# Optimization experiments

Measured on AMD Instinct MI355X. Metric: run time of the kernel, lower is better.

The kernel has to match this reference:

```python
import jax, jax.numpy as jnp
import numpy as np

D_MODEL = 2048
NUM_HEADS = 16
D_K = D_MODEL // NUM_HEADS
B, S, PAST = 2, 1024, 3072


def setup_inputs() -> dict:
    key = jax.random.key(0)
    ks = jax.random.split(key, 12)
    s = 1.0 / np.sqrt(D_MODEL)
    inp = {
        "x": jax.random.normal(ks[0], (B, S, D_MODEL), dtype=jnp.float32),
        "past_key": jax.random.normal(ks[1], (B, NUM_HEADS, PAST, D_K), dtype=jnp.float32),
        "past_value": jax.random.normal(ks[2], (B, NUM_HEADS, PAST, D_K), dtype=jnp.float32),
        "Wq": jax.random.normal(ks[3], (D_MODEL, D_MODEL), dtype=jnp.float32) * s,
        "bq": jax.random.normal(ks[4], (D_MODEL,), dtype=jnp.float32) * s,
        "Wk": jax.random.normal(ks[5], (D_MODEL, D_MODEL), dtype=jnp.float32) * s,
        "bk": jax.random.normal(ks[6], (D_MODEL,), dtype=jnp.float32) * s,
        "Wv": jax.random.normal(ks[7], (D_MODEL, D_MODEL), dtype=jnp.float32) * s,
        "bv": jax.random.normal(ks[8], (D_MODEL,), dtype=jnp.float32) * s,
        "Wo": jax.random.normal(ks[9], (D_MODEL, D_MODEL), dtype=jnp.float32) * s,
        "bo": jax.random.normal(ks[10], (D_MODEL,), dtype=jnp.float32) * s,
    }
    return inp


def reference(x, past_key, past_value, Wq, bq, Wk, bk, Wv, bv, Wo, bo):
    b, s, _ = x.shape
    # torch nn.Linear: y = x @ W^T + b
    def proj(W, bias):
        y = jnp.einsum('bsd,ed->bse', x, W) + bias
        return y.reshape(b, s, NUM_HEADS, D_K).transpose(0, 2, 1, 3)  # [B,H,S,dk]
    Q = proj(Wq, bq)
    K = proj(Wk, bk)
    V = proj(Wv, bv)
    K = jnp.concatenate([past_key, K], axis=2)   # [B,H,PAST+S,dk]
    V = jnp.concatenate([past_value, V], axis=2)
    scale = 1.0 / np.sqrt(D_K).astype(np.float32)
    scores = jnp.einsum('bhqd,bhkd->bhqk', Q, K) * scale
    attn = jax.nn.softmax(scores, axis=-1)
    out = jnp.einsum('bhqk,bhkd->bhqd', attn, V)          # [B,H,S,dk]
    out = out.transpose(0, 2, 1, 3).reshape(b, s, D_MODEL)
    out = jnp.einsum('bsd,ed->bse', out, Wo) + bo
    return out, K, V
```

## Files before the change

### kernel.cpp

```cpp
#include <hip/hip_runtime.h>
#include <stdint.h>

typedef __bf16 bf16;
typedef __bf16 bf16x4 __attribute__((ext_vector_type(4)));
typedef __bf16 bf16x8 __attribute__((ext_vector_type(8)));
typedef float  f32x4  __attribute__((ext_vector_type(4)));

#define DMODEL 2048
#define NH 16
#define DK 128
#define SS 1024
#define PASTLEN 3072
#define LTOT 4096
#define KVTILES 64
#define NSPLIT 4
#define NT 16

__device__ __forceinline__ void gload16(const void* g, void* l) {
    __builtin_amdgcn_global_load_lds(
        (__attribute__((address_space(1))) void*)(uintptr_t)g,
        (__attribute__((address_space(3))) void*)(uintptr_t)l,
        16, 0, 0);
}

__global__ __launch_bounds__(256) void cvt5_k(
    const float* __restrict__ s0, const float* __restrict__ s1,
    const float* __restrict__ s2, const float* __restrict__ s3,
    const float* __restrict__ s4,
    bf16* __restrict__ d0, bf16* __restrict__ d1, bf16* __restrict__ d2,
    bf16* __restrict__ d3, bf16* __restrict__ d4, int n8)
{
    const float* s; bf16* d;
    switch (blockIdx.y) {
        case 0: s = s0; d = d0; break;
        case 1: s = s1; d = d1; break;
        case 2: s = s2; d = d2; break;
        case 3: s = s3; d = d3; break;
        default: s = s4; d = d4; break;
    }
    int stride = gridDim.x * blockDim.x;
    for (int i = blockIdx.x*blockDim.x + threadIdx.x; i < n8; i += stride) {
        const float4* p = (const float4*)s + (size_t)i*2;
        float4 a = p[0], b = p[1];
        bf16x8 o;
        o[0]=(bf16)a.x; o[1]=(bf16)a.y; o[2]=(bf16)a.z; o[3]=(bf16)a.w;
        o[4]=(bf16)b.x; o[5]=(bf16)b.y; o[6]=(bf16)b.z; o[7]=(bf16)b.w;
        *((bf16x8*)d + i) = o;
    }
}

__global__ __launch_bounds__(256) void gemm_bt(
    const bf16* __restrict__ A,
    const bf16* __restrict__ W0, const bf16* __restrict__ W1, const bf16* __restrict__ W2,
    const float* __restrict__ b0, const float* __restrict__ b1, const float* __restrict__ b2,
    bf16* __restrict__ outQ, float* __restrict__ outK, float* __restrict__ outV,
    float* __restrict__ outO,
    const float* __restrict__ pk, const float* __restrict__ pv,
    bf16* __restrict__ Kbb, bf16* __restrict__ Vbb, int mode)
{
    __shared__ __align__(16) char lds[34816];
    const int tid  = threadIdx.x;

    if (mode == 0 && blockIdx.x >= 768) {
        float* Vt_f = (float*)lds;
        const int pp  = blockIdx.x - 768;
        const int tau = pp % 48, bh = pp / 48;
        const float* srcK = pk + ((size_t)bh*PASTLEN + tau*64)*DK;
        const float* srcV = pv + ((size_t)bh*PASTLEN + tau*64)*DK;
        float* dstKf = outK + ((size_t)bh*LTOT + tau*64)*DK;
        float* dstVf = outV + ((size_t)bh*LTOT + tau*64)*DK;
        char* kblob = (char*)Kbb + (((size_t)bh*KVTILES + tau) << 14);
        char* vblob = (char*)Vbb + (((size_t)bh*KVTILES + tau) << 14);
        #pragma unroll
        for (int i = 0; i < 8; ++i) {
            const int f4 = i*256 + tid;
            const int r  = f4 >> 5;
            const int c8 = f4 & 31;
            float4 k4 = ((const float4*)srcK)[f4];
            float4 v4 = ((const float4*)srcV)[f4];
            ((float4*)dstKf)[f4] = k4;
            ((float4*)dstVf)[f4] = v4;
            bf16x4 kq; kq[0]=(bf16)k4.x; kq[1]=(bf16)k4.y; kq[2]=(bf16)k4.z; kq[3]=(bf16)k4.w;
            *(bf16x4*)(kblob + r*256 + ((c8*8) ^ ((r&7)<<4))) = kq;
            *(float4*)&Vt_f[r*132 + c8*4] = v4;
        }
        __syncthreads();
        const int d = tid >> 1, half = tid & 1;
        const int dx = (d & 7) << 4;
        #pragma unroll
        for (int jj = 0; jj < 4; ++jj) {
            const int chunk = half*4 + jj;
            bf16x8 o;
            #pragma unroll
            for (int e = 0; e < 8; ++e) {
                const int j  = chunk*8 + e;
                const int oe = (j & 32) + ((j & 4) << 2) + (((j >> 3) & 3) << 2) + (j & 3);
                o[e] = (bf16)Vt_f[oe*132 + d];
            }
            *(bf16x8*)(vblob + d*128 + ((chunk*16) ^ dx)) = o;
        }
        return;
    }

    bf16* As = (bf16*)lds;
    bf16* Bs = (bf16*)(lds + 8192);
    const int wave = tid >> 6, lane = tid & 63;
    const int l15 = lane & 15, l4 = lane >> 4;
    int which, ntile, mt;
    if (mode == 0) {
        mt = blockIdx.x & 15;
        const int ny = blockIdx.x >> 4;
        which = ny >> 4; ntile = ny & 15;
    } else {
        mt = blockIdx.x; which = 3; ntile = blockIdx.y;
    }
    const bf16*  W    = (mode != 0 || which == 0) ? W0 : (which == 1 ? W1 : W2);
    const float* bias = (mode != 0 || which == 0) ? b0 : (which == 1 ? b1 : b2);
    const int m0 = mt * 128, n0 = ntile * 128;
    const int wm = wave >> 1, wn = wave & 1;

    f32x4 acc[4][4] = {};

    for (int k0 = 0; k0 < DMODEL; k0 += 32) {
        __syncthreads();
        #pragma unroll
        for (int c = 0; c < 2; ++c) {
            const int base = c*4096 + wave*1024;
            const int byte = base + lane*16;
            const int row  = byte >> 6;
            const int ke   = (byte & 63) >> 1;
            gload16(A + (size_t)(m0+row)*DMODEL + k0 + ke, (char*)As + base);
            gload16(W + (size_t)(n0+row)*DMODEL + k0 + ke, (char*)Bs + base);
        }
        asm volatile("s_waitcnt vmcnt(0)" ::: "memory");
        __syncthreads();
        bf16x8 af[4], bfv[4];
        #pragma unroll
        for (int mf = 0; mf < 4; ++mf)
            af[mf] = *(const bf16x8*)((const char*)As + (wm*64 + mf*16 + l15)*64 + l4*16);
        #pragma unroll
        for (int nf = 0; nf < 4; ++nf)
            bfv[nf] = *(const bf16x8*)((const char*)Bs + (wn*64 + nf*16 + l15)*64 + l4*16);
        #pragma unroll
        for (int mf = 0; mf < 4; ++mf)
            #pragma unroll
            for (int nf = 0; nf < 4; ++nf)
                acc[mf][nf] = __builtin_amdgcn_mfma_f32_16x16x32_bf16(af[mf], bfv[nf], acc[mf][nf], 0, 0, 0);
    }

    float bv4[4];
    #pragma unroll
    for (int nf = 0; nf < 4; ++nf) bv4[nf] = bias[n0 + wn*64 + nf*16 + l15];

    const int rbase = m0 + wm*64 + l4*4;
    const int cbase = n0 + wn*64 + l15;

    if (mode == 1) {
        #pragma unroll
        for (int mf = 0; mf < 4; ++mf)
        #pragma unroll
        for (int nf = 0; nf < 4; ++nf) {
            const int col = cbase + nf*16;
            #pragma unroll
            for (int r = 0; r < 4; ++r) {
                const int row = rbase + mf*16 + r;
                outO[(size_t)row*DMODEL + col] = acc[mf][nf][r] + bv4[nf];
            }
        }
    } else if (which == 0) {
        const float qs = 0.08838834764831845f * 1.4426950408889634f;
        #pragma unroll
        for (int mf = 0; mf < 4; ++mf)
        #pragma unroll
        for (int nf = 0; nf < 4; ++nf) {
            const int col = cbase + nf*16;
            const int h = col >> 7, d = col & 127;
            #pragma unroll
            for (int r = 0; r < 4; ++r) {
                const int row = rbase + mf*16 + r;
                const int b = row >> 10, s = row & 1023;
                outQ[((size_t)(b*NH + h)*SS + s)*DK + d] = (bf16)((acc[mf][nf][r] + bv4[nf]) * qs);
            }
        }
    } else {
        float* dst = (which == 1) ? outK : outV;
        #pragma unroll
        for (int mf = 0; mf < 4; ++mf)
        #pragma unroll
        for (int nf = 0; nf < 4; ++nf) {
            const int col = cbase + nf*16;
            const int h = col >> 7, d = col & 127;
            #pragma unroll
            for (int r = 0; r < 4; ++r) {
                const int row = rbase + mf*16 + r;
                const int b = row >> 10, s = row & 1023;
                dst[((size_t)(b*NH + h)*LTOT + PASTLEN + s)*DK + d] = acc[mf][nf][r] + bv4[nf];
            }
        }
    }
}

__global__ __launch_bounds__(256) void kvprep_new(
    const float* __restrict__ Kf, const float* __restrict__ Vf,
    bf16* __restrict__ Kb, bf16* __restrict__ Vb)
{
    __shared__ float Vt_f[64*132];
    const int tid = threadIdx.x;
    const int tau = 48 + blockIdx.x, bh = blockIdx.y;
    const float* srcK = Kf + ((size_t)bh*LTOT + tau*64)*DK;
    const float* srcV = Vf + ((size_t)bh*LTOT + tau*64)*DK;
    char* kblob = (char*)Kb + (((size_t)bh*KVTILES + tau) << 14);
    char* vblob = (char*)Vb + (((size_t)bh*KVTILES + tau) << 14);

    #pragma unroll
    for (int i = 0; i < 8; ++i) {
        const int f4 = i*256 + tid;
        const int r  = f4 >> 5;
        const int c8 = f4 & 31;
        float4 k4 = ((const float4*)srcK)[f4];
        float4 v4 = ((const float4*)srcV)[f4];
        bf16x4 kq; kq[0]=(bf16)k4.x; kq[1]=(bf16)k4.y; kq[2]=(bf16)k4.z; kq[3]=(bf16)k4.w;
        *(bf16x4*)(kblob + r*256 + ((c8*8) ^ ((r&7)<<4))) = kq;
        *(float4*)&Vt_f[r*132 + c8*4] = v4;
    }
    __syncthreads();
    const int d = tid >> 1, half = tid & 1;
    const int dx = (d & 7) << 4;
    #pragma unroll
    for (int jj = 0; jj < 4; ++jj) {
        const int chunk = half*4 + jj;
        bf16x8 o;
        #pragma unroll
        for (int e = 0; e < 8; ++e) {
            const int j  = chunk*8 + e;
            const int oe = (j & 32) + ((j & 4) << 2) + (((j >> 3) & 3) << 2) + (j & 3);
            o[e] = (bf16)Vt_f[oe*132 + d];
        }
        *(bf16x8*)(vblob + d*128 + ((chunk*16) ^ dx)) = o;
    }
}

__global__ __launch_bounds__(512, 2) void attn_k(
    const bf16* __restrict__ Qb,
    const bf16* __restrict__ Kb, const bf16* __restrict__ Vb,
    bf16* __restrict__ Opart, float* __restrict__ Marr, float* __restrict__ Larr)
{
    __shared__ __align__(16) char KL[4][16384];
    __shared__ __align__(16) char VL[4][16384];

    const int tid  = threadIdx.x;
    const int wave = tid >> 6, lane = tid & 63;
    const int l15 = lane & 15, l4 = lane >> 4;
    const int wgid = blockIdx.x;
    const int qt = (wgid >> 3) & 3;
    const int g  = ((wgid >> 5) << 3) | (wgid & 7);
    const int bh = g >> 2, sp = g & 3;
    const int qbase = qt*256 + wave*32;

    bf16x8 qf[2][4];
    #pragma unroll
    for (int qq = 0; qq < 2; ++qq) {
        const bf16* qptr = Qb + ((size_t)bh*SS + qbase + qq*16 + l15)*DK;
        #pragma unroll
        for (int ks = 0; ks < 4; ++ks)
            qf[qq][ks] = *(const bf16x8*)(qptr + ks*32 + l4*8);
    }

    const char* kblobs = (const char*)Kb + (((size_t)bh*KVTILES + sp*NT) << 14);
    const char* vblobs = (const char*)Vb + (((size_t)bh*KVTILES + sp*NT) << 14);
    const int soff = wave*2048;

    bf16x8 ones8;
    #pragma unroll
    for (int e = 0; e < 8; ++e) ones8[e] = (bf16)1.0f;

    float m_run[2];
    f32x4 oacc[2][8];
    f32x4 lacc[2];
    m_run[0] = -1e30f; m_run[1] = -1e30f;
    #pragma unroll
    for (int qq = 0; qq < 2; ++qq) {
        #pragma unroll
        for (int df = 0; df < 8; ++df) oacc[qq][df] = f32x4{0.f,0.f,0.f,0.f};
        lacc[qq] = f32x4{0.f,0.f,0.f,0.f};
    }

    #pragma unroll
    for (int tt = 0; tt < 2; ++tt)
        #pragma unroll
        for (int c = 0; c < 2; ++c) {
            gload16(kblobs + ((size_t)tt << 14) + soff + c*1024 + lane*16, KL[tt] + soff + c*1024);
            gload16(vblobs + ((size_t)tt << 14) + soff + c*1024 + lane*16, VL[tt] + soff + c*1024);
        }

    for (int t = 0; t < NT; ++t) {
        const int cur = t & 3;
        if (t + 2 < NT) {
            const int nb = (t + 2) & 3;
            const char* kb = kblobs + ((size_t)(t+2) << 14);
            const char* vb = vblobs + ((size_t)(t+2) << 14);
            #pragma unroll
            for (int c = 0; c < 2; ++c) {
                gload16(kb + soff + c*1024 + lane*16, KL[nb] + soff + c*1024);
                gload16(vb + soff + c*1024 + lane*16, VL[nb] + soff + c*1024);
            }
            asm volatile("s_waitcnt vmcnt(8)" ::: "memory");
        } else if (t + 1 < NT) {
            asm volatile("s_waitcnt vmcnt(4)" ::: "memory");
        } else {
            asm volatile("s_waitcnt vmcnt(0)" ::: "memory");
        }
        __builtin_amdgcn_s_barrier();

        const char* Kc = KL[cur];
        const char* Vc = VL[cur];

        f32x4 sa[2][4];
        #pragma unroll
        for (int qq = 0; qq < 2; ++qq)
            #pragma unroll
            for (int nf = 0; nf < 4; ++nf) sa[qq][nf] = f32x4{0.f,0.f,0.f,0.f};
        __builtin_amdgcn_s_setprio(1);
        #pragma unroll
        for (int nf = 0; nf < 4; ++nf) {
            const int krow = nf*16 + l15;
            const int rx = (krow & 7) << 4;
            #pragma unroll
            for (int ks = 0; ks < 4; ++ks) {
                bf16x8 kf = *(const bf16x8*)(Kc + krow*256 + ((ks*64 + l4*16) ^ rx));
                sa[0][nf] = __builtin_amdgcn_mfma_f32_16x16x32_bf16(kf, qf[0][ks], sa[0][nf], 0,0,0);
                sa[1][nf] = __builtin_amdgcn_mfma_f32_16x16x32_bf16(kf, qf[1][ks], sa[1][nf], 0,0,0);
            }
        }
        __builtin_amdgcn_s_setprio(0);

        float mt2[2];
        #pragma unroll
        for (int qq = 0; qq < 2; ++qq) {
            float a0 = fmaxf(fmaxf(sa[qq][0][0], sa[qq][0][1]), fmaxf(sa[qq][0][2], sa[qq][0][3]));
            float a1 = fmaxf(fmaxf(sa[qq][1][0], sa[qq][1][1]), fmaxf(sa[qq][1][2], sa[qq][1][3]));
            float a2 = fmaxf(fmaxf(sa[qq][2][0], sa[qq][2][1]), fmaxf(sa[qq][2][2], sa[qq][2][3]));
            float a3 = fmaxf(fmaxf(sa[qq][3][0], sa[qq][3][1]), fmaxf(sa[qq][3][2], sa[qq][3][3]));
            float v = fmaxf(fmaxf(a0, a1), fmaxf(a2, a3));
            v = fmaxf(v, __shfl_xor(v, 16, 64));
            v = fmaxf(v, __shfl_xor(v, 32, 64));
            mt2[qq] = v;
        }
        const bool ok = (mt2[0] <= m_run[0] + 8.0f) && (mt2[1] <= m_run[1] + 8.0f);
        if (!__all(ok)) {
            #pragma unroll
            for (int qq = 0; qq < 2; ++qq) {
                const float mn   = fmaxf(m_run[qq], mt2[qq]);
                const float corr = exp2f(m_run[qq] - mn);
                m_run[qq] = mn;
                #pragma unroll
                for (int r = 0; r < 4; ++r) {
                    const float c = __shfl(corr, (lane & 48) | (l4*4 + r), 64);
                    lacc[qq][r] *= c;
                    #pragma unroll
                    for (int df = 0; df < 8; ++df) oacc[qq][df][r] *= c;
                }
            }
        }

        bf16x8 pf[2][2];
        #pragma unroll
        for (int qq = 0; qq < 2; ++qq)
            #pragma unroll
            for (int ks2 = 0; ks2 < 2; ++ks2) {
                bf16x8 v;
                #pragma unroll
                for (int e = 0; e < 8; ++e)
                    v[e] = (bf16)exp2f(sa[qq][ks2*2 + (e >> 2)][e & 3] - m_run[qq]);
                pf[qq][ks2] = v;
            }

        __builtin_amdgcn_s_setprio(1);
        #pragma unroll
        for (int ks2 = 0; ks2 < 2; ++ks2) {
            lacc[0] = __builtin_amdgcn_mfma_f32_16x16x32_bf16(pf[0][ks2], ones8, lacc[0], 0,0,0);
            lacc[1] = __builtin_amdgcn_mfma_f32_16x16x32_bf16(pf[1][ks2], ones8, lacc[1], 0,0,0);
            #pragma unroll
            for (int df = 0; df < 8; ++df) {
                const int d = df*16 + l15;
                bf16x8 vf = *(const bf16x8*)(Vc + d*128 + ((ks2*64 + l4*16) ^ ((d&7)<<4)));
                oacc[0][df] = __builtin_amdgcn_mfma_f32_16x16x32_bf16(pf[0][ks2], vf, oacc[0][df], 0,0,0);
                oacc[1][df] = __builtin_amdgcn_mfma_f32_16x16x32_bf16(pf[1][ks2], vf, oacc[1][df], 0,0,0);
            }
        }
        __builtin_amdgcn_s_setprio(0);
    }

    bf16* op = Opart + ((size_t)sp*32 + bh)*SS*DK;
    #pragma unroll
    for (int qq = 0; qq < 2; ++qq)
        #pragma unroll
        for (int df = 0; df < 8; ++df)
            #pragma unroll
            for (int r = 0; r < 4; ++r) {
                const int q = qbase + qq*16 + l4*4 + r;
                op[(size_t)q*DK + df*16 + l15] = (bf16)oacc[qq][df][r];
            }
    if (l4 == 0) {
        #pragma unroll
        for (int qq = 0; qq < 2; ++qq)
            Marr[(size_t)sp*32768 + bh*SS + qbase + qq*16 + l15] = m_run[qq];
    }
    if (l15 == 0) {
        #pragma unroll
        for (int qq = 0; qq < 2; ++qq)
            #pragma unroll
            for (int r = 0; r < 4; ++r) {
                const int q = qbase + qq*16 + l4*4 + r;
                Larr[(size_t)sp*32768 + bh*SS + q] = lacc[qq][r];
            }
    }
}

__global__ __launch_bounds__(256) void combine_k(
    const bf16* __restrict__ Opart, const float* __restrict__ Marr,
    const float* __restrict__ Larr, bf16* __restrict__ Ob)
{
    const int gid = blockIdx.x*256 + threadIdx.x;
    const int row = gid >> 4;
    const int c8  = gid & 15;
    const int bh = row >> 10, q = row & 1023;
    float m[NSPLIT], l[NSPLIT];
    #pragma unroll
    for (int s = 0; s < NSPLIT; ++s) {
        m[s] = Marr[(size_t)s*32768 + row];
        l[s] = Larr[(size_t)s*32768 + row];
    }
    float M = m[0];
    #pragma unroll
    for (int s = 1; s < NSPLIT; ++s) M = fmaxf(M, m[s]);
    float w[NSPLIT], den = 0.f;
    #pragma unroll
    for (int s = 0; s < NSPLIT; ++s) { w[s] = exp2f(m[s] - M); den += l[s]*w[s]; }
    const float inv = 1.f / den;
    #pragma unroll
    for (int s = 0; s < NSPLIT; ++s) w[s] *= inv;
    float acc[8] = {};
    #pragma unroll
    for (int s = 0; s < NSPLIT; ++s) {
        bf16x8 p = *(const bf16x8*)(Opart + (size_t)s*4194304 + (size_t)row*DK + c8*8);
        #pragma unroll
        for (int e = 0; e < 8; ++e) acc[e] += (float)p[e]*w[s];
    }
    const int b = bh >> 4, h = bh & 15;
    bf16x8 o;
    #pragma unroll
    for (int e = 0; e < 8; ++e) o[e] = (bf16)acc[e];
    *(bf16x8*)(Ob + ((size_t)(b*SS + q))*DMODEL + h*DK + c8*8) = o;
}

extern "C" void kernel_launch(void* const* d_in, const int* in_sizes, int n_in,
                              void* d_out, int out_size, void* d_ws, size_t ws_size,
                              hipStream_t stream) {
    const float* x  = (const float*)d_in[0];
    const float* pk = (const float*)d_in[1];
    const float* pv = (const float*)d_in[2];
    const float* Wq = (const float*)d_in[3];
    const float* bq = (const float*)d_in[4];
    const float* Wk = (const float*)d_in[5];
    const float* bk = (const float*)d_in[6];
    const float* Wv = (const float*)d_in[7];
    const float* bv = (const float*)d_in[8];
    const float* Wo = (const float*)d_in[9];
    const float* bo = (const float*)d_in[10];

    float* out  = (float*)d_out;
    float* Kout = out + 4194304;
    float* Vout = out + 20971520;

    char* ws = (char*)d_ws;
    bf16* xb    = (bf16*)(ws);
    bf16* Wqb   = (bf16*)(ws + (size_t)8*1024*1024);
    bf16* Wkb   = (bf16*)(ws + (size_t)16*1024*1024);
    bf16* Wvb   = (bf16*)(ws + (size_t)24*1024*1024);
    bf16* Wob   = (bf16*)(ws + (size_t)32*1024*1024);
    bf16* Qb    = (bf16*)(ws + (size_t)40*1024*1024);
    bf16* Ob    = (bf16*)(ws + (size_t)48*1024*1024);
    bf16* Kb    = (bf16*)(ws + (size_t)56*1024*1024);
    bf16* Vb    = (bf16*)(ws + (size_t)88*1024*1024);
    bf16*  Opart = (bf16*)(ws);
    float* Marr  = out;
    float* Larr  = out + 131072;

    cvt5_k<<<dim3(1024, 5), 256, 0, stream>>>(x, Wq, Wk, Wv, Wo,
                                              xb, Wqb, Wkb, Wvb, Wob, 524288);
    gemm_bt<<<2304, 256, 0, stream>>>(xb, Wqb, Wkb, Wvb, bq, bk, bv,
                                      Qb, Kout, Vout, nullptr,
                                      pk, pv, Kb, Vb, 0);
    kvprep_new<<<dim3(16, 32), 256, 0, stream>>>(Kout, Vout, Kb, Vb);
    attn_k<<<512, 512, 0, stream>>>(Qb, Kb, Vb, Opart, Marr, Larr);
    combine_k<<<2048, 256, 0, stream>>>(Opart, Marr, Larr, Ob);
    gemm_bt<<<dim3(16, 16), 256, 0, stream>>>(Ob, Wob, nullptr, nullptr, bo, nullptr, nullptr,
                                              nullptr, nullptr, nullptr, out,
                                              nullptr, nullptr, nullptr, nullptr, 1);
}
```

Baseline: 289.6 us.

## Halve attention KV splits, interleave KV-copy blocks with GEMM blocks, shrink LDS

The attention split-K factor drops from 4 to 2, so each workgroup walks 32 KV tiles and the attention grid shrinks from 512 to 256 blocks. This cuts partial-output traffic and combine work, but it also reduces parallelism. In the fused QKV GEMM launch, past-KV copy/convert blocks are now interleaved with GEMM tiles (two copy blocks per GEMM block) instead of trailing them. The V transpose is done in two 64-column halves, which roughly halves LDS use for the gemm and kvprep kernels and should allow higher occupancy, at the cost of an extra barrier pair.

```diff
diff --git a/kernel.cpp b/kernel.cpp
--- a/kernel.cpp
+++ b/kernel.cpp
@@ -13,8 +13,8 @@
 #define PASTLEN 3072
 #define LTOT 4096
 #define KVTILES 64
-#define NSPLIT 4
-#define NT 16
+#define NSPLIT 2
+#define NT 32
 
 __device__ __forceinline__ void gload16(const void* g, void* l) {
     __builtin_amdgcn_global_load_lds(
@@ -58,46 +58,57 @@
     const float* __restrict__ pk, const float* __restrict__ pv,
     bf16* __restrict__ Kbb, bf16* __restrict__ Vbb, int mode)
 {
-    __shared__ __align__(16) char lds[34816];
+    __shared__ __align__(16) char lds[16896];
     const int tid  = threadIdx.x;
 
-    if (mode == 0 && blockIdx.x >= 768) {
-        float* Vt_f = (float*)lds;
-        const int pp  = blockIdx.x - 768;
-        const int tau = pp % 48, bh = pp / 48;
+    if (mode == 0 && (blockIdx.x % 3) != 0) {
+        const int gi  = blockIdx.x;
+        const int pid = (gi/3)*2 + (gi%3) - 1;
+        const int tau = pid % 48, bh = pid / 48;
         const float* srcK = pk + ((size_t)bh*PASTLEN + tau*64)*DK;
         const float* srcV = pv + ((size_t)bh*PASTLEN + tau*64)*DK;
         float* dstKf = outK + ((size_t)bh*LTOT + tau*64)*DK;
         float* dstVf = outV + ((size_t)bh*LTOT + tau*64)*DK;
         char* kblob = (char*)Kbb + (((size_t)bh*KVTILES + tau) << 14);
         char* vblob = (char*)Vbb + (((size_t)bh*KVTILES + tau) << 14);
+
         #pragma unroll
         for (int i = 0; i < 8; ++i) {
             const int f4 = i*256 + tid;
-            const int r  = f4 >> 5;
-            const int c8 = f4 & 31;
+            const int r = f4 >> 5, c8 = f4 & 31;
             float4 k4 = ((const float4*)srcK)[f4];
-            float4 v4 = ((const float4*)srcV)[f4];
             ((float4*)dstKf)[f4] = k4;
-            ((float4*)dstVf)[f4] = v4;
             bf16x4 kq; kq[0]=(bf16)k4.x; kq[1]=(bf16)k4.y; kq[2]=(bf16)k4.z; kq[3]=(bf16)k4.w;
             *(bf16x4*)(kblob + r*256 + ((c8*8) ^ ((r&7)<<4))) = kq;
-            *(float4*)&Vt_f[r*132 + c8*4] = v4;
-        }
-        __syncthreads();
-        const int d = tid >> 1, half = tid & 1;
-        const int dx = (d & 7) << 4;
-        #pragma unroll
-        for (int jj = 0; jj < 4; ++jj) {
-            const int chunk = half*4 + jj;
-            bf16x8 o;
-            #pragma unroll
-            for (int e = 0; e < 8; ++e) {
-                const int j  = chunk*8 + e;
-                const int oe = (j & 32) + ((j & 4) << 2) + (((j >> 3) & 3) << 2) + (j & 3);
-                o[e] = (bf16)Vt_f[oe*132 + d];
-            }
-            *(bf16x8*)(vblob + d*128 + ((chunk*16) ^ dx)) = o;
+        }
+        float* Vt_f = (float*)lds;
+        #pragma unroll
+        for (int half = 0; half < 2; ++half) {
+            __syncthreads();
+            #pragma unroll
+            for (int i = 0; i < 4; ++i) {
+                const int f4 = i*256 + tid;
+                const int r = f4 >> 4, c4 = f4 & 15;
+                float4 v4 = ((const float4*)srcV)[r*32 + half*16 + c4];
+                ((float4*)dstVf)[r*32 + half*16 + c4] = v4;
+                *(float4*)&Vt_f[r*66 + c4*4] = v4;
+            }
+            __syncthreads();
+            #pragma unroll
+            for (int w = 0; w < 2; ++w) {
+                const int idx = w*256 + tid;
+                const int dd = idx >> 3;
+                const int d  = half*64 + dd;
+                const int chunk = idx & 7;
+                bf16x8 o;
+                #pragma unroll
+                for (int e = 0; e < 8; ++e) {
+                    const int j  = chunk*8 + e;
+                    const int oe = (j & 32) + ((j & 4) << 2) + (((j >> 3) & 3) << 2) + (j & 3);
+                    o[e] = (bf16)Vt_f[oe*66 + dd];
+                }
+                *(bf16x8*)(vblob + d*128 + ((chunk*16) ^ ((d&7)<<4))) = o;
+            }
         }
         return;
     }
@@ -108,8 +119,9 @@
     const int l15 = lane & 15, l4 = lane >> 4;
     int which, ntile, mt;
     if (mode == 0) {
-        mt = blockIdx.x & 15;
-        const int ny = blockIdx.x >> 4;
+        const int id = blockIdx.x / 3;
+        mt = id & 15;
+        const int ny = id >> 4;
         which = ny >> 4; ntile = ny & 15;
     } else {
         mt = blockIdx.x; which = 3; ntile = blockIdx.y;
@@ -204,7 +216,7 @@
     const float* __restrict__ Kf, const float* __restrict__ Vf,
     bf16* __restrict__ Kb, bf16* __restrict__ Vb)
 {
-    __shared__ float Vt_f[64*132];
+    __shared__ float Vt_f[64*66];
     const int tid = threadIdx.x;
     const int tau = 48 + blockIdx.x, bh = blockIdx.y;
     const float* srcK = Kf + ((size_t)bh*LTOT + tau*64)*DK;
@@ -215,28 +227,37 @@
     #pragma unroll
     for (int i = 0; i < 8; ++i) {
         const int f4 = i*256 + tid;
-        const int r  = f4 >> 5;
-        const int c8 = f4 & 31;
+        const int r = f4 >> 5, c8 = f4 & 31;
         float4 k4 = ((const float4*)srcK)[f4];
-        float4 v4 = ((const float4*)srcV)[f4];
         bf16x4 kq; kq[0]=(bf16)k4.x; kq[1]=(bf16)k4.y; kq[2]=(bf16)k4.z; kq[3]=(bf16)k4.w;
         *(bf16x4*)(kblob + r*256 + ((c8*8) ^ ((r&7)<<4))) = kq;
-        *(float4*)&Vt_f[r*132 + c8*4] = v4;
-    }
-    __syncthreads();
-    const int d = tid >> 1, half = tid & 1;
-    const int dx = (d & 7) << 4;
-    #pragma unroll
-    for (int jj = 0; jj < 4; ++jj) {
-        const int chunk = half*4 + jj;
-        bf16x8 o;
-        #pragma unroll
-        for (int e = 0; e < 8; ++e) {
-            const int j  = chunk*8 + e;
-            const int oe = (j & 32) + ((j & 4) << 2) + (((j >> 3) & 3) << 2) + (j & 3);
-            o[e] = (bf16)Vt_f[oe*132 + d];
-        }
-        *(bf16x8*)(vblob + d*128 + ((chunk*16) ^ dx)) = o;
+    }
+    #pragma unroll
+    for (int half = 0; half < 2; ++half) {
+        __syncthreads();
+        #pragma unroll
+        for (int i = 0; i < 4; ++i) {
+            const int f4 = i*256 + tid;
+            const int r = f4 >> 4, c4 = f4 & 15;
+            float4 v4 = ((const float4*)srcV)[r*32 + half*16 + c4];
+            *(float4*)&Vt_f[r*66 + c4*4] = v4;
+        }
+        __syncthreads();
+        #pragma unroll
+        for (int w = 0; w < 2; ++w) {
+            const int idx = w*256 + tid;
+            const int dd = idx >> 3;
+            const int d  = half*64 + dd;
+            const int chunk = idx & 7;
+            bf16x8 o;
+            #pragma unroll
+            for (int e = 0; e < 8; ++e) {
+                const int j  = chunk*8 + e;
+                const int oe = (j & 32) + ((j & 4) << 2) + (((j >> 3) & 3) << 2) + (j & 3);
+                o[e] = (bf16)Vt_f[oe*66 + dd];
+            }
+            *(bf16x8*)(vblob + d*128 + ((chunk*16) ^ ((d&7)<<4))) = o;
+        }
     }
 }
 
@@ -254,7 +275,7 @@
     const int wgid = blockIdx.x;
     const int qt = (wgid >> 3) & 3;
     const int g  = ((wgid >> 5) << 3) | (wgid & 7);
-    const int bh = g >> 2, sp = g & 3;
+    const int bh = g >> 1, sp = g & 1;
     const int qbase = qt*256 + wave*32;
 
     bf16x8 qf[2][4];
@@ -486,14 +507,14 @@
     bf16*  Opart = (bf16*)(ws);
     float* Marr  = out;
     float* Larr  = out + 131072;
-
+    
     cvt5_k<<<dim3(1024, 5), 256, 0, stream>>>(x, Wq, Wk, Wv, Wo,
                                               xb, Wqb, Wkb, Wvb, Wob, 524288);
     gemm_bt<<<2304, 256, 0, stream>>>(xb, Wqb, Wkb, Wvb, bq, bk, bv,
                                       Qb, Kout, Vout, nullptr,
                                       pk, pv, Kb, Vb, 0);
     kvprep_new<<<dim3(16, 32), 256, 0, stream>>>(Kout, Vout, Kb, Vb);
-    attn_k<<<512, 512, 0, stream>>>(Qb, Kb, Vb, Opart, Marr, Larr);
+    attn_k<<<256, 512, 0, stream>>>(Qb, Kb, Vb, Opart, Marr, Larr);
     combine_k<<<2048, 256, 0, stream>>>(Opart, Marr, Larr, Ob);
     gemm_bt<<<dim3(16, 16), 256, 0, stream>>>(Ob, Wob, nullptr, nullptr, bo, nullptr, nullptr,
                                               nullptr, nullptr, nullptr, out,
```

New measurement: 295.1 us. About the same (+1.9%).
